# Kernel optimization log

Measured on AMD Instinct MI355X. Metric: run time of the kernel, lower is better.

## Reference

```python
import jax, jax.numpy as jnp
import numpy as np

D, H, HD, FF, L, SYM, B = 256, 8, 32, 256, 3, 64, 32768


def setup_inputs() -> dict:
    key = jax.random.key(0)
    ks = iter(jax.random.split(key, 32))
    n = lambda shape, s=0.02: jax.random.normal(next(ks), shape, dtype=jnp.float32) * s
    return {
        "global_emb": n((B, D), 1.0),
        "pert_emb": n((B, D), 1.0),
        "sym_feat": n((B, SYM), 1.0),
        "ppi_feat": n((B, D), 1.0),
        "sym_W": n((SYM, D)),
        "sym_b": jnp.zeros((D,), jnp.float32),
        "sym_ln_g": jnp.ones((D,), jnp.float32),
        "sym_ln_b": jnp.zeros((D,), jnp.float32),
        "token_type_emb": n((4, D)),
        "Wqkv": n((L, D, 3 * D)),
        "bqkv": jnp.zeros((L, 3 * D), jnp.float32),
        "Wo": n((L, D, D)),
        "bo": jnp.zeros((L, D), jnp.float32),
        "ln1_g": jnp.ones((L, D), jnp.float32),
        "ln1_b": jnp.zeros((L, D), jnp.float32),
        "ln2_g": jnp.ones((L, D), jnp.float32),
        "ln2_b": jnp.zeros((L, D), jnp.float32),
        "W1": n((L, D, FF)),
        "b1": jnp.zeros((L, FF), jnp.float32),
        "W2": n((L, FF, D)),
        "b2": jnp.zeros((L, D), jnp.float32),
        "final_ln_g": jnp.ones((D,), jnp.float32),
        "final_ln_b": jnp.zeros((D,), jnp.float32),
        "out_ln_g": jnp.ones((D,), jnp.float32),
        "out_ln_b": jnp.zeros((D,), jnp.float32),
    }


def _ln(x, g, b, eps=1e-5):
    m = jnp.mean(x, axis=-1, keepdims=True)
    v = jnp.mean(jnp.square(x - m), axis=-1, keepdims=True)
    return (x - m) * jax.lax.rsqrt(v + eps) * g + b


def reference(global_emb, pert_emb, sym_feat, ppi_feat, sym_W, sym_b, sym_ln_g,
              sym_ln_b, token_type_emb, Wqkv, bqkv, Wo, bo, ln1_g, ln1_b,
              ln2_g, ln2_b, W1, b1, W2, b2, final_ln_g, final_ln_b,
              out_ln_g, out_ln_b):
    # sym projection + LN, then stack 4 tokens and add token-type embedding
    sym_proj = _ln(sym_feat @ sym_W + sym_b, sym_ln_g, sym_ln_b)
    x = jnp.stack([global_emb, pert_emb, sym_proj, ppi_feat], axis=1)  # [B,4,D]
    x = x + token_type_emb[None]
    Bsz = x.shape[0]
    scale = 1.0 / np.sqrt(HD).astype(np.float32)
    for l in range(L):  # pre-norm TransformerEncoderLayer x3 (eval: dropout off)
        h = _ln(x, ln1_g[l], ln1_b[l])
        qkv = h @ Wqkv[l] + bqkv[l]  # [B,4,3D]
        q, k, v = jnp.split(qkv, 3, axis=-1)
        q = q.reshape(Bsz, 4, H, HD).transpose(0, 2, 1, 3)  # [B,H,4,HD]
        k = k.reshape(Bsz, 4, H, HD).transpose(0, 2, 1, 3)
        v = v.reshape(Bsz, 4, H, HD).transpose(0, 2, 1, 3)
        attn = jax.nn.softmax(jnp.einsum("bhqd,bhkd->bhqk", q, k) * scale, axis=-1)
        o = jnp.einsum("bhqk,bhkd->bhqd", attn, v)
        o = o.transpose(0, 2, 1, 3).reshape(Bsz, 4, D)
        x = x + (o @ Wo[l] + bo[l])
        h2 = _ln(x, ln2_g[l], ln2_b[l])
        ff = jax.nn.gelu(h2 @ W1[l] + b1[l], approximate=False) @ W2[l] + b2[l]
        x = x + ff
    x = _ln(x, final_ln_g, final_ln_b)  # TransformerEncoder final norm
    return _ln(jnp.mean(x, axis=1), out_ln_g, out_ln_b)  # mean over 4 tokens + out_norm
```

## Files before the change

kernel.cpp:

```cpp
#include <hip/hip_runtime.h>
#include <hip/hip_bf16.h>
#include <math.h>

typedef unsigned short u16;
typedef __attribute__((ext_vector_type(8))) short v8s;
typedef __attribute__((ext_vector_type(4))) short v4s;
typedef __attribute__((ext_vector_type(4))) float v4f;

__device__ __forceinline__ float bf2f(u16 u){
  union { float f; unsigned int i; } v; v.i = ((unsigned int)u) << 16; return v.f;
}
__device__ __forceinline__ u16 f2bf(float f){
  union { __hip_bfloat16 h; u16 u; } cv; cv.h = __float2bfloat16(f); return cv.u;
}
__device__ __forceinline__ bool det_bf16(const void* p){
  return ((const u16*)p)[0] != 0;
}
__device__ __forceinline__ float ldp(const void* p, size_t i, bool bf){
  return bf ? bf2f(((const u16*)p)[i]) : ((const float*)p)[i];
}
__device__ __forceinline__ void ld8f(const void* p, size_t i, bool bf, float* o){
  if (bf){
    v8s a = *(const v8s*)((const u16*)p + i);
    #pragma unroll
    for (int j=0;j<8;j++) o[j]=bf2f((u16)a[j]);
  } else {
    const float4* q=(const float4*)((const float*)p + i);
    float4 a=q[0], b=q[1];
    o[0]=a.x;o[1]=a.y;o[2]=a.z;o[3]=a.w;o[4]=b.x;o[5]=b.y;o[6]=b.z;o[7]=b.w;
  }
}
__device__ __forceinline__ void ld4f(const void* p, size_t i, bool bf, float* o){
  if (bf){
    v4s a = *(const v4s*)((const u16*)p + i);
    #pragma unroll
    for (int j=0;j<4;j++) o[j]=bf2f((u16)a[j]);
  } else {
    float4 q = *(const float4*)((const float*)p + i);
    o[0]=q.x;o[1]=q.y;o[2]=q.z;o[3]=q.w;
  }
}

#define MFMA(a,b,c) __builtin_amdgcn_mfma_f32_16x16x32_bf16((a),(b),(c),0,0,0)

template<int CTRL>
__device__ __forceinline__ float dpp_qp(float x){
  union { float f; int i; } u; u.f = x;
  u.i = __builtin_amdgcn_mov_dpp(u.i, CTRL, 0xF, 0xF, true);
  return u.f;
}

__device__ __forceinline__ int swz(int row, int col, int stride){
  return row*stride + ((((col>>3) ^ (row&7))<<3) | (col&7));
}

__device__ __forceinline__ void st4(u16* dst, v4f a, const float* b){
  v4s o;
  #pragma unroll
  for (int i=0;i<4;i++) o[i] = (short)f2bf(a[i] + b[i]);
  *(v4s*)dst = o;
}
__device__ __forceinline__ void rmw4(u16* p, v4f a, const float* b){
  v4s x = *(v4s*)p; v4s o;
  #pragma unroll
  for (int i=0;i<4;i++) o[i] = (short)f2bf(bf2f((u16)x[i]) + a[i] + b[i]);
  *(v4s*)p = o;
}

__device__ __forceinline__ float gelu_f(float u){
  float ax = fabsf(u)*0.70710678118f;
  float t = 1.f/(1.f + 0.3275911f*ax);
  float y = t*(0.254829592f + t*(-0.284496736f + t*(1.421413741f +
            t*(-1.453152027f + t*1.061405429f))));
  float er = 1.f - y*__expf(-ax*ax);
  er = copysignf(er, u);
  return 0.5f*u*(1.f + er);
}

__global__ __launch_bounds__(64) void repack_kernel(
    const void* __restrict__ symW, const void* __restrict__ Wqkv,
    const void* __restrict__ Wo, const void* __restrict__ W1, const void* __restrict__ W2,
    const void* __restrict__ ln1g, const void* __restrict__ ln1b,
    const void* __restrict__ ln2g, const void* __restrict__ ln2b,
    const void* __restrict__ bqkv, const void* __restrict__ b1,
    u16* __restrict__ wf_sym, u16* __restrict__ wf_qkv, u16* __restrict__ wf_o,
    u16* __restrict__ wf_1, u16* __restrict__ wf_2,
    float* __restrict__ cq1, float* __restrict__ cq0,
    float* __restrict__ cf1, float* __restrict__ cf0,
    const void* __restrict__ dtp)
{
  bool bf = det_bf16(dtp);
  int idx = blockIdx.x;
  int ln = threadIdx.x;

  if (idx >= 2336){
    int i2 = idx - 2336;
    int lay = i2 >> 4, r2 = i2 & 15;
    const void *Wp, *g, *be, *bb; size_t woff, goff, boff; int N, n; float *o1, *o0;
    if (r2 < 12){
      n = r2*64 + ln; N = 768; Wp = Wqkv; woff = (size_t)lay*196608;
      g = ln1g; be = ln1b; bb = bqkv; goff = (size_t)lay*256; boff = (size_t)lay*768;
      o1 = cq1 + lay*768; o0 = cq0 + lay*768;
    } else {
      int rr = r2 - 12; n = rr*64 + ln; N = 256; Wp = W1; woff = (size_t)lay*65536;
      g = ln2g; be = ln2b; bb = b1; goff = (size_t)lay*256; boff = (size_t)lay*256;
      o1 = cf1 + lay*256; o0 = cf0 + lay*256;
    }
    float a1 = 0.f, a0 = 0.f;
    for (int k = 0; k < 256; k++){
      float wv = ldp(Wp, woff + (size_t)k*N + n, bf);
      a1 += bf2f(f2bf(ldp(g, goff+k, bf) * wv));
      a0 += ldp(be, goff+k, bf) * wv;
    }
    o1[n] = a1;
    o0[n] = a0 + ldp(bb, boff + n, bf);
    return;
  }

  const void* src; u16* dst; int N, kb, nb; size_t soff;
  const void* gscale = nullptr; size_t gsoff = 0;
  if (idx < 32) { src = symW; dst = wf_sym; N = 256; kb = idx >> 4; nb = idx & 15; soff = 0; }
  else {
    idx -= 32;
    int lay = idx / 768, r = idx % 768;
    if (r < 384) { N = 768; src = Wqkv; soff = (size_t)lay*196608; dst = wf_qkv + lay*196608; kb = r/48; nb = r%48;
                   gscale = ln1g; gsoff = (size_t)lay*256; }
    else {
      r -= 384; int which = r >> 7, rr = r & 127; N = 256; kb = rr >> 4; nb = rr & 15;
      soff = (size_t)lay*65536;
      if (which == 0)      { src = Wo; dst = wf_o + lay*65536; }
      else if (which == 1) { src = W1; dst = wf_1 + lay*65536; gscale = ln2g; gsoff = (size_t)lay*256; }
      else                 { src = W2; dst = wf_2 + lay*65536; }
    }
  }
  int n  = nb*16 + (ln & 15);
  int k0 = kb*32 + (ln >> 4)*8;
  u16* d = dst + (((size_t)(kb*(N>>4) + nb))*64 + ln)*8;
  #pragma unroll
  for (int j = 0; j < 8; j++){
    float sc = gscale ? ldp(gscale, gsoff + k0 + j, bf) : 1.f;
    d[j] = f2bf(sc * ldp(src, soff + (size_t)(k0+j)*N + n, bf));
  }
}

__device__ __forceinline__ void ln64s(const u16* src, u16* dst,
    const void* gp, const void* bp, size_t goff, bool bf, int t)
{
  int r = t>>3, p = t&7;
  float vv[32];
  float su=0.f, sq=0.f;
  #pragma unroll
  for (int k4=0;k4<4;k4++){
    v8s a = *(const v8s*)(src + swz(r, p*32+k4*8, 256));
    #pragma unroll
    for (int j=0;j<8;j++){ float v=bf2f((u16)a[j]); vv[k4*8+j]=v; su+=v; sq+=v*v; }
  }
  su += dpp_qp<0xB1>(su); sq += dpp_qp<0xB1>(sq);
  su += dpp_qp<0x4E>(su); sq += dpp_qp<0x4E>(sq);
  su += __shfl_xor(su,4); sq += __shfl_xor(sq,4);
  float m = su*(1.f/256.f);
  float rs = rsqrtf(sq*(1.f/256.f) - m*m + 1e-5f);
  #pragma unroll
  for (int k4=0;k4<4;k4++){
    float gg[8], bb[8];
    ld8f(gp, goff + p*32 + k4*8, bf, gg);
    ld8f(bp, goff + p*32 + k4*8, bf, bb);
    v8s o;
    #pragma unroll
    for (int j=0;j<8;j++) o[j]=(short)f2bf((vv[k4*8+j]-m)*rs*gg[j]+bb[j]);
    *(v8s*)(dst + swz(r, p*32+k4*8, 256)) = o;
  }
}

__device__ __forceinline__ void mrs64(const u16* src, float* dst, int t){
  int r = t>>3, p = t&7;
  float su=0.f, sq=0.f;
  #pragma unroll
  for (int k4=0;k4<4;k4++){
    v8s a = *(const v8s*)(src + swz(r, p*32+k4*8, 256));
    #pragma unroll
    for (int j=0;j<8;j++){ float v=bf2f((u16)a[j]); su+=v; sq+=v*v; }
  }
  su += dpp_qp<0xB1>(su); sq += dpp_qp<0xB1>(sq);
  su += dpp_qp<0x4E>(su); sq += dpp_qp<0x4E>(sq);
  su += __shfl_xor(su,4); sq += __shfl_xor(sq,4);
  float m = su*(1.f/256.f);
  float rs = rsqrtf(sq*(1.f/256.f) - m*m + 1e-5f);
  if (p == 0){ dst[2*r] = m; dst[2*r+1] = rs; }
}

__global__ __launch_bounds__(512,4) void fused_kernel(
    const void* __restrict__ gemb, const void* __restrict__ pemb,
    const void* __restrict__ symf, const void* __restrict__ ppi,
    const void* __restrict__ symb, const void* __restrict__ slng,
    const void* __restrict__ slnb, const void* __restrict__ tte,
    const void* __restrict__ bo, const void* __restrict__ b2p,
    const void* __restrict__ flng, const void* __restrict__ flnb,
    const void* __restrict__ olng, const void* __restrict__ olnb,
    const float* __restrict__ cq1, const float* __restrict__ cq0,
    const float* __restrict__ cf1, const float* __restrict__ cf0,
    const u16* __restrict__ wf_sym, const u16* __restrict__ wf_qkv,
    const u16* __restrict__ wf_o, const u16* __restrict__ wf_1,
    const u16* __restrict__ wf_2,
    void* __restrict__ out)
{
  __shared__ __align__(16) u16 X[16384];
  __shared__ __align__(16) u16 H[16384];
  __shared__ __align__(16) u16 symst[1024];
  __shared__ __align__(8)  float mrsA[128];
  __shared__ __align__(8)  float mrsB[128];

  bool bf = det_bf16(slng);
  int t = threadIdx.x;
  int w = t>>6, ln = t&63, quad = ln>>4, c = ln&15;
  int row0 = blockIdx.x * 64;
  int S0 = row0 >> 2;

  {
    if (t < 128){
      int r = t>>3, pp = t&7;
      float tmp[8];
      ld8f(symf, (size_t)(S0+r)*64 + pp*8, bf, tmp);
      v8s o;
      #pragma unroll
      for (int j=0;j<8;j++) o[j]=(short)f2bf(tmp[j]);
      *(v8s*)(symst + swz(r, pp*8, 64)) = o;
    } else {
      int u = t-128;
      int rid = u>>3, p = u&7;
      int s = rid/3, z = rid - s*3;
      int tok = (z==2)?3:z;
      const void* src = (z==0)?gemb: (z==1)?pemb: ppi;
      #pragma unroll
      for (int k4=0;k4<4;k4++){
        float a8[8], t8[8];
        ld8f(src, (size_t)(S0+s)*256 + p*32 + k4*8, bf, a8);
        ld8f(tte, (size_t)tok*256 + p*32 + k4*8, bf, t8);
        v8s o;
        #pragma unroll
        for (int j=0;j<8;j++) o[j]=(short)f2bf(a8[j]+t8[j]);
        *(v8s*)(X + swz(s*4+tok, p*32+k4*8, 256)) = o;
      }
    }
    __syncthreads();
    {
      v4f acc[2];
      v4f z4={0.f,0.f,0.f,0.f};
      acc[0]=z4; acc[1]=z4;
      #pragma unroll
      for (int kb=0;kb<2;kb++){
        v8s a = *(const v8s*)(symst + swz(c, kb*32+quad*8, 64));
        #pragma unroll
        for (int j=0;j<2;j++){
          v8s b = *(const v8s*)(wf_sym + (((size_t)(kb*16+w*2+j))*64+ln)*8);
          acc[j] = MFMA(b, a, acc[j]);
        }
      }
      #pragma unroll
      for (int j=0;j<2;j++){
        int colb = (w*2+j)*16 + quad*4;
        float sb[4]; ld4f(symb, colb, bf, sb);
        st4(H + swz(c, colb, 256), acc[j], sb);
      }
    }
    __syncthreads();
    if (t < 128){
      int r = t>>3, p = t&7;
      float vv[32];
      float su=0.f, sq=0.f;
      #pragma unroll
      for (int k4=0;k4<4;k4++){
        v8s a = *(const v8s*)(H + swz(r, p*32+k4*8, 256));
        #pragma unroll
        for (int j=0;j<8;j++){ float v=bf2f((u16)a[j]); vv[k4*8+j]=v; su+=v; sq+=v*v; }
      }
      su += dpp_qp<0xB1>(su); sq += dpp_qp<0xB1>(sq);
      su += dpp_qp<0x4E>(su); sq += dpp_qp<0x4E>(sq);
      su += __shfl_xor(su,4); sq += __shfl_xor(sq,4);
      float m = su*(1.f/256.f);
      float rs = rsqrtf(sq*(1.f/256.f) - m*m + 1e-5f);
      #pragma unroll
      for (int k4=0;k4<4;k4++){
        float gg[8], bb[8], t8[8];
        ld8f(slng, p*32+k4*8, bf, gg);
        ld8f(slnb, p*32+k4*8, bf, bb);
        ld8f(tte, 512 + p*32+k4*8, bf, t8);
        v8s o;
        #pragma unroll
        for (int j=0;j<8;j++) o[j]=(short)f2bf((vv[k4*8+j]-m)*rs*gg[j]+bb[j]+t8[j]);
        *(v8s*)(X + swz(r*4+2, p*32+k4*8, 256)) = o;
      }
    }
    __syncthreads();
  }

  #pragma unroll 1
  for (int lay = 0; lay < 3; lay++){

    mrs64(X, mrsA, t);

    {
      const u16* wq = wf_qkv + (size_t)lay*196608;
      int h = w;
      v4f z4={0.f,0.f,0.f,0.f};
      const float scl = 0.17677669529663687f;
      v4f s01[2], s23[2];
      auto qkdots = [&](int hf, v4f* sout){
        v4f Qa[2][2], Ka[2][2];
        #pragma unroll
        for (int m2=0;m2<2;m2++){ Qa[m2][0]=z4;Qa[m2][1]=z4;Ka[m2][0]=z4;Ka[m2][1]=z4; }
        #pragma unroll 2
        for (int kb=0;kb<8;kb++){
          v8s Bq0 = *(const v8s*)(wq + (((size_t)(kb*48      + h*2  ))*64+ln)*8);
          v8s Bq1 = *(const v8s*)(wq + (((size_t)(kb*48      + h*2+1))*64+ln)*8);
          v8s Bk0 = *(const v8s*)(wq + (((size_t)(kb*48 + 16 + h*2  ))*64+ln)*8);
          v8s Bk1 = *(const v8s*)(wq + (((size_t)(kb*48 + 16 + h*2+1))*64+ln)*8);
          #pragma unroll
          for (int m2=0;m2<2;m2++){
            v8s a = *(const v8s*)(X + swz((hf*2+m2)*16+c, kb*32+quad*8, 256));
            Qa[m2][0]=MFMA(Bq0,a,Qa[m2][0]);
            Qa[m2][1]=MFMA(Bq1,a,Qa[m2][1]);
            Ka[m2][0]=MFMA(Bk0,a,Ka[m2][0]);
            Ka[m2][1]=MFMA(Bk1,a,Ka[m2][1]);
          }
        }
        if (hf == 0) __syncthreads();
        v4f q1[2], q0[2], k1[2], k0f[2];
        #pragma unroll
        for (int jj=0;jj<2;jj++){
          int d0 = lay*768 + h*32 + jj*16 + quad*4;
          q1[jj]  = *(const v4f*)(cq1 + d0);
          q0[jj]  = *(const v4f*)(cq0 + d0);
          k1[jj]  = *(const v4f*)(cq1 + d0 + 256);
          k0f[jj] = *(const v4f*)(cq0 + d0 + 256);
        }
        #pragma unroll
        for (int m2=0;m2<2;m2++){
          float2 mr = *(const float2*)&mrsA[2*((hf*2+m2)*16 + c)];
          float q8[8], k8[8];
          #pragma unroll
          for (int jj=0;jj<2;jj++)
            #pragma unroll
            for (int i=0;i<4;i++){
              q8[jj*4+i] = mr.y*(Qa[m2][jj][i] - mr.x*q1[jj][i]) + q0[jj][i];
              k8[jj*4+i] = mr.y*(Ka[m2][jj][i] - mr.x*k1[jj][i]) + k0f[jj][i];
            }
          float sp0=0.f, sp1=0.f, sp2=0.f, sp3=0.f;
          #pragma unroll
          for (int x=0;x<8;x++){
            sp0 += q8[x]*k8[x];
            sp1 += q8[x]*dpp_qp<0xB1>(k8[x]);
            sp2 += q8[x]*dpp_qp<0x4E>(k8[x]);
            sp3 += q8[x]*dpp_qp<0x1B>(k8[x]);
          }
          sp0 += __shfl_xor(sp0,16); sp0 += __shfl_xor(sp0,32);
          sp1 += __shfl_xor(sp1,16); sp1 += __shfl_xor(sp1,32);
          sp2 += __shfl_xor(sp2,16); sp2 += __shfl_xor(sp2,32);
          sp3 += __shfl_xor(sp3,16); sp3 += __shfl_xor(sp3,32);
          v4f s; s[0]=sp0*scl; s[1]=sp1*scl; s[2]=sp2*scl; s[3]=sp3*scl;
          sout[m2] = s;
        }
      };
      qkdots(0, s01);
      __builtin_amdgcn_sched_barrier(0);
      qkdots(1, s23);
      v4f p0, p1, p2, p3;
      {
        auto smax = [&](v4f s)->v4f{
          float mx = fmaxf(fmaxf(s[0],s[1]),fmaxf(s[2],s[3]));
          float e0=__expf(s[0]-mx), e1=__expf(s[1]-mx), e2=__expf(s[2]-mx), e3=__expf(s[3]-mx);
          float inv = 1.f/(e0+e1+e2+e3);
          v4f p; p[0]=e0*inv; p[1]=e1*inv; p[2]=e2*inv; p[3]=e3*inv;
          return p;
        };
        p0 = smax(s01[0]); p1 = smax(s01[1]); p2 = smax(s23[0]); p3 = smax(s23[1]);
      }
      v4f Va[4][2];
      #pragma unroll
      for (int mb=0;mb<4;mb++){ Va[mb][0]=z4; Va[mb][1]=z4; }
      #pragma unroll 2
      for (int kb=0;kb<8;kb++){
        v8s Bv0 = *(const v8s*)(wq + (((size_t)(kb*48 + 32 + h*2  ))*64+ln)*8);
        v8s Bv1 = *(const v8s*)(wq + (((size_t)(kb*48 + 32 + h*2+1))*64+ln)*8);
        #pragma unroll
        for (int mb=0;mb<4;mb++){
          v8s a = *(const v8s*)(X + swz(mb*16+c, kb*32+quad*8, 256));
          Va[mb][0]=MFMA(Bv0,a,Va[mb][0]);
          Va[mb][1]=MFMA(Bv1,a,Va[mb][1]);
        }
      }
      {
        v4f v1[2], v0[2];
        #pragma unroll
        for (int jj=0;jj<2;jj++){
          int d0 = lay*768 + 512 + h*32 + jj*16 + quad*4;
          v1[jj] = *(const v4f*)(cq1 + d0);
          v0[jj] = *(const v4f*)(cq0 + d0);
        }
        #pragma unroll
        for (int mb=0;mb<4;mb++){
          float2 mr = *(const float2*)&mrsA[2*(mb*16 + c)];
          #pragma unroll
          for (int jj=0;jj<2;jj++)
            #pragma unroll
            for (int i=0;i<4;i++)
              Va[mb][jj][i] = mr.y*(Va[mb][jj][i] - mr.x*v1[jj][i]) + v0[jj][i];
        }
      }
      #pragma unroll
      for (int mb=0;mb<4;mb++){
        v4f P = (mb==0)?p0:(mb==1)?p1:(mb==2)?p2:p3;
        #pragma unroll
        for (int jj=0;jj<2;jj++){
          v4f o;
          #pragma unroll
          for (int i=0;i<4;i++){
            float v = Va[mb][jj][i];
            float r = P[0]*v;
            r += P[1]*dpp_qp<0xB1>(v);
            r += P[2]*dpp_qp<0x4E>(v);
            r += P[3]*dpp_qp<0x1B>(v);
            o[i] = r;
          }
          v4s pk;
          #pragma unroll
          for (int i=0;i<4;i++) pk[i]=(short)f2bf(o[i]);
          *(v4s*)(H + swz(mb*16+c, h*32 + jj*16 + quad*4, 256)) = pk;
        }
      }
    }
    __syncthreads();

    {
      const u16* wo = wf_o + (size_t)lay*65536;
      v4f acc[4][2];
      v4f z4={0.f,0.f,0.f,0.f};
      #pragma unroll
      for (int mb=0;mb<4;mb++){ acc[mb][0]=z4; acc[mb][1]=z4; }
      #pragma unroll 2
      for (int kb=0;kb<8;kb++){
        v8s B0 = *(const v8s*)(wo + (((size_t)(kb*16 + w*2  ))*64+ln)*8);
        v8s B1 = *(const v8s*)(wo + (((size_t)(kb*16 + w*2+1))*64+ln)*8);
        #pragma unroll
        for (int mb=0;mb<4;mb++){
          v8s a = *(const v8s*)(H + swz(mb*16+c, kb*32+quad*8, 256));
          acc[mb][0]=MFMA(B0,a,acc[mb][0]);
          acc[mb][1]=MFMA(B1,a,acc[mb][1]);
        }
      }
      #pragma unroll
      for (int jj=0;jj<2;jj++){
        int colb = (w*2+jj)*16 + quad*4;
        float bs[4]; ld4f(bo, (size_t)lay*256 + colb, bf, bs);
        #pragma unroll
        for (int mb=0;mb<4;mb++)
          rmw4(X + swz(mb*16+c, colb, 256), acc[mb][jj], bs);
      }
    }
    __syncthreads();

    mrs64(X, mrsB, t);

    {
      const u16* w1 = wf_1 + (size_t)lay*65536;
      v4f acc[4][2];
      v4f z4={0.f,0.f,0.f,0.f};
      #pragma unroll
      for (int mb=0;mb<4;mb++){ acc[mb][0]=z4; acc[mb][1]=z4; }
      #pragma unroll 2
      for (int kb=0;kb<8;kb++){
        v8s B0 = *(const v8s*)(w1 + (((size_t)(kb*16 + w*2  ))*64+ln)*8);
        v8s B1 = *(const v8s*)(w1 + (((size_t)(kb*16 + w*2+1))*64+ln)*8);
        #pragma unroll
        for (int mb=0;mb<4;mb++){
          v8s a = *(const v8s*)(X + swz(mb*16+c, kb*32+quad*8, 256));
          acc[mb][0]=MFMA(B0,a,acc[mb][0]);
          acc[mb][1]=MFMA(B1,a,acc[mb][1]);
        }
      }
      __syncthreads();
      #pragma unroll
      for (int jj=0;jj<2;jj++){
        int colb = (w*2+jj)*16 + quad*4;
        v4f f1 = *(const v4f*)(cf1 + lay*256 + colb);
        v4f f0 = *(const v4f*)(cf0 + lay*256 + colb);
        #pragma unroll
        for (int mb=0;mb<4;mb++){
          float2 mr = *(const float2*)&mrsB[2*(mb*16 + c)];
          v4s pk;
          #pragma unroll
          for (int i=0;i<4;i++){
            float val = mr.y*(acc[mb][jj][i] - mr.x*f1[i]) + f0[i];
            pk[i]=(short)f2bf(gelu_f(val));
          }
          *(v4s*)(H + swz(mb*16+c, colb, 256)) = pk;
        }
      }
    }
    __syncthreads();

    {
      const u16* w2 = wf_2 + (size_t)lay*65536;
      v4f acc[4][2];
      v4f z4={0.f,0.f,0.f,0.f};
      #pragma unroll
      for (int mb=0;mb<4;mb++){ acc[mb][0]=z4; acc[mb][1]=z4; }
      #pragma unroll 2
      for (int kb=0;kb<8;kb++){
        v8s B0 = *(const v8s*)(w2 + (((size_t)(kb*16 + w*2  ))*64+ln)*8);
        v8s B1 = *(const v8s*)(w2 + (((size_t)(kb*16 + w*2+1))*64+ln)*8);
        #pragma unroll
        for (int mb=0;mb<4;mb++){
          v8s a = *(const v8s*)(H + swz(mb*16+c, kb*32+quad*8, 256));
          acc[mb][0]=MFMA(B0,a,acc[mb][0]);
          acc[mb][1]=MFMA(B1,a,acc[mb][1]);
        }
      }
      #pragma unroll
      for (int jj=0;jj<2;jj++){
        int colb = (w*2+jj)*16 + quad*4;
        float bs[4]; ld4f(b2p, (size_t)lay*256 + colb, bf, bs);
        #pragma unroll
        for (int mb=0;mb<4;mb++)
          rmw4(X + swz(mb*16+c, colb, 256), acc[mb][jj], bs);
      }
    }
    __syncthreads();
  }

  ln64s(X, H, flng, flnb, 0, bf, t);
  __syncthreads();
  if (t < 128){
    int s = t>>3, p = t&7;
    float y[32];
    #pragma unroll
    for (int j=0;j<32;j++) y[j]=0.f;
    #pragma unroll
    for (int r4=0;r4<4;r4++)
      #pragma unroll
      for (int k4=0;k4<4;k4++){
        v8s a = *(const v8s*)(H + swz(s*4+r4, p*32+k4*8, 256));
        #pragma unroll
        for (int j=0;j<8;j++) y[k4*8+j] += bf2f((u16)a[j]);
      }
    float su=0.f, sq=0.f;
    #pragma unroll
    for (int j=0;j<32;j++){ y[j]*=0.25f; su+=y[j]; sq+=y[j]*y[j]; }
    su += dpp_qp<0xB1>(su); sq += dpp_qp<0xB1>(sq);
    su += dpp_qp<0x4E>(su); sq += dpp_qp<0x4E>(sq);
    su += __shfl_xor(su,4); sq += __shfl_xor(sq,4);
    float m = su*(1.f/256.f);
    float rs = rsqrtf(sq*(1.f/256.f) - m*m + 1e-5f);
    #pragma unroll
    for (int k4=0;k4<4;k4++){
      float gg[8], bb[8];
      ld8f(olng, p*32+k4*8, bf, gg);
      ld8f(olnb, p*32+k4*8, bf, bb);
      if (bf){
        u16* dst = (u16*)out + (size_t)(S0+s)*256 + p*32 + k4*8;
        v8s o;
        #pragma unroll
        for (int j=0;j<8;j++) o[j]=(short)f2bf((y[k4*8+j]-m)*rs*gg[j]+bb[j]);
        *(v8s*)dst = o;
      } else {
        float* dst = (float*)out + (size_t)(S0+s)*256 + p*32 + k4*8;
        #pragma unroll
        for (int j=0;j<8;j++) dst[j] = (y[k4*8+j]-m)*rs*gg[j]+bb[j];
      }
    }
  }
}

extern "C" void kernel_launch(void* const* d_in, const int* in_sizes, int n_in,
                              void* d_out, int out_size, void* d_ws, size_t ws_size,
                              hipStream_t stream)
{
  const void* gemb=d_in[0];
  const void* pemb=d_in[1];
  const void* symf=d_in[2];
  const void* ppi =d_in[3];
  const void* symW=d_in[4];
  const void* symb=d_in[5];
  const void* slng=d_in[6];
  const void* slnb=d_in[7];
  const void* tte =d_in[8];
  const void* Wqkv=d_in[9];
  const void* bqkv=d_in[10];
  const void* Wo  =d_in[11];
  const void* bo  =d_in[12];
  const void* ln1g=d_in[13];
  const void* ln1b=d_in[14];
  const void* ln2g=d_in[15];
  const void* ln2b=d_in[16];
  const void* W1  =d_in[17];
  const void* b1  =d_in[18];
  const void* W2  =d_in[19];
  const void* b2  =d_in[20];
  const void* flng=d_in[21];
  const void* flnb=d_in[22];
  const void* olng=d_in[23];
  const void* olnb=d_in[24];

  u16* wf_sym=(u16*)d_ws;
  u16* wf_qkv=wf_sym + 16384;
  u16* wf_o  =wf_qkv + 589824;
  u16* wf_1  =wf_o  + 196608;
  u16* wf_2  =wf_1  + 196608;
  float* cq1 = (float*)(wf_2 + 196608);
  float* cq0 = cq1 + 2304;
  float* cf1 = cq0 + 2304;
  float* cf0 = cf1 + 768;

  repack_kernel<<<2384,64,0,stream>>>(symW,Wqkv,Wo,W1,W2,
      ln1g,ln1b,ln2g,ln2b,bqkv,b1,
      wf_sym,wf_qkv,wf_o,wf_1,wf_2, cq1,cq0,cf1,cf0, slng);
  fused_kernel<<<2048,512,0,stream>>>(
      gemb,pemb,symf,ppi,symb,slng,slnb,tte,bo,b2,
      flng,flnb,olng,olnb, cq1,cq0,cf1,cf0,
      wf_sym,wf_qkv,wf_o,wf_1,wf_2, d_out);
}
```

Baseline: 727.8 us.

## Halve block tile to 32 rows with 4 waves, each wave covering more columns

After: 1.033 ms. 41.9% more time.

```diff
diff --git a/kernel.cpp b/kernel.cpp
--- a/kernel.cpp
+++ b/kernel.cpp
@@ -143,7 +143,7 @@
   }
 }
 
-__device__ __forceinline__ void ln64s(const u16* src, u16* dst,
+__device__ __forceinline__ void ln32s(const u16* src, u16* dst,
     const void* gp, const void* bp, size_t goff, bool bf, int t)
 {
   int r = t>>3, p = t&7;
@@ -172,7 +172,7 @@
   }
 }
 
-__device__ __forceinline__ void mrs64(const u16* src, float* dst, int t){
+__device__ __forceinline__ void mrs32(const u16* src, float* dst, int t){
   int r = t>>3, p = t&7;
   float su=0.f, sq=0.f;
   #pragma unroll
@@ -189,7 +189,7 @@
   if (p == 0){ dst[2*r] = m; dst[2*r+1] = rs; }
 }
 
-__global__ __launch_bounds__(512,4) void fused_kernel(
+__global__ __launch_bounds__(256,4) void fused_kernel(
     const void* __restrict__ gemb, const void* __restrict__ pemb,
     const void* __restrict__ symf, const void* __restrict__ ppi,
     const void* __restrict__ symb, const void* __restrict__ slng,
@@ -204,20 +204,20 @@
     const u16* __restrict__ wf_2,
     void* __restrict__ out)
 {
-  __shared__ __align__(16) u16 X[16384];
-  __shared__ __align__(16) u16 H[16384];
+  __shared__ __align__(16) u16 X[8192];
+  __shared__ __align__(16) u16 H[8192];
   __shared__ __align__(16) u16 symst[1024];
-  __shared__ __align__(8)  float mrsA[128];
-  __shared__ __align__(8)  float mrsB[128];
+  __shared__ __align__(8)  float mrsA[64];
+  __shared__ __align__(8)  float mrsB[64];
 
   bool bf = det_bf16(slng);
   int t = threadIdx.x;
   int w = t>>6, ln = t&63, quad = ln>>4, c = ln&15;
-  int row0 = blockIdx.x * 64;
+  int row0 = blockIdx.x * 32;
   int S0 = row0 >> 2;
 
   {
-    if (t < 128){
+    if (t < 64){
       int r = t>>3, pp = t&7;
       float tmp[8];
       ld8f(symf, (size_t)(S0+r)*64 + pp*8, bf, tmp);
@@ -226,7 +226,7 @@
       for (int j=0;j<8;j++) o[j]=(short)f2bf(tmp[j]);
       *(v8s*)(symst + swz(r, pp*8, 64)) = o;
     } else {
-      int u = t-128;
+      int u = t-64;
       int rid = u>>3, p = u&7;
       int s = rid/3, z = rid - s*3;
       int tok = (z==2)?3:z;
@@ -244,27 +244,30 @@
     }
     __syncthreads();
     {
-      v4f acc[2];
+      v4f acc[4];
       v4f z4={0.f,0.f,0.f,0.f};
-      acc[0]=z4; acc[1]=z4;
+      #pragma unroll
+      for (int j=0;j<4;j++) acc[j]=z4;
       #pragma unroll
       for (int kb=0;kb<2;kb++){
         v8s a = *(const v8s*)(symst + swz(c, kb*32+quad*8, 64));
         #pragma unroll
-        for (int j=0;j<2;j++){
-          v8s b = *(const v8s*)(wf_sym + (((size_t)(kb*16+w*2+j))*64+ln)*8);
+        for (int j=0;j<4;j++){
+          v8s b = *(const v8s*)(wf_sym + (((size_t)(kb*16+w*4+j))*64+ln)*8);
           acc[j] = MFMA(b, a, acc[j]);
         }
       }
-      #pragma unroll
-      for (int j=0;j<2;j++){
-        int colb = (w*2+j)*16 + quad*4;
-        float sb[4]; ld4f(symb, colb, bf, sb);
-        st4(H + swz(c, colb, 256), acc[j], sb);
+      if (c < 8){
+        #pragma unroll
+        for (int j=0;j<4;j++){
+          int colb = (w*4+j)*16 + quad*4;
+          float sb[4]; ld4f(symb, colb, bf, sb);
+          st4(H + swz(c, colb, 256), acc[j], sb);
+        }
       }
     }
     __syncthreads();
-    if (t < 128){
+    if (t < 64){
       int r = t>>3, p = t&7;
       float vv[32];
       float su=0.f, sq=0.f;
@@ -297,15 +300,14 @@
   #pragma unroll 1
   for (int lay = 0; lay < 3; lay++){
 
-    mrs64(X, mrsA, t);
+    mrs32(X, mrsA, t);
 
     {
       const u16* wq = wf_qkv + (size_t)lay*196608;
-      int h = w;
       v4f z4={0.f,0.f,0.f,0.f};
       const float scl = 0.17677669529663687f;
-      v4f s01[2], s23[2];
-      auto qkdots = [&](int hf, v4f* sout){
+      v4f s0h[2], s1h[2];
+      auto qkdots = [&](int h, bool bar, v4f* sout){
         v4f Qa[2][2], Ka[2][2];
         #pragma unroll
         for (int m2=0;m2<2;m2++){ Qa[m2][0]=z4;Qa[m2][1]=z4;Ka[m2][0]=z4;Ka[m2][1]=z4; }
@@ -317,14 +319,14 @@
           v8s Bk1 = *(const v8s*)(wq + (((size_t)(kb*48 + 16 + h*2+1))*64+ln)*8);
           #pragma unroll
           for (int m2=0;m2<2;m2++){
-            v8s a = *(const v8s*)(X + swz((hf*2+m2)*16+c, kb*32+quad*8, 256));
+            v8s a = *(const v8s*)(X + swz(m2*16+c, kb*32+quad*8, 256));
             Qa[m2][0]=MFMA(Bq0,a,Qa[m2][0]);
             Qa[m2][1]=MFMA(Bq1,a,Qa[m2][1]);
             Ka[m2][0]=MFMA(Bk0,a,Ka[m2][0]);
             Ka[m2][1]=MFMA(Bk1,a,Ka[m2][1]);
           }
         }
-        if (hf == 0) __syncthreads();
+        if (bar) __syncthreads();
         v4f q1[2], q0[2], k1[2], k0f[2];
         #pragma unroll
         for (int jj=0;jj<2;jj++){
@@ -336,7 +338,7 @@
         }
         #pragma unroll
         for (int m2=0;m2<2;m2++){
-          float2 mr = *(const float2*)&mrsA[2*((hf*2+m2)*16 + c)];
+          float2 mr = *(const float2*)&mrsA[2*(m2*16 + c)];
           float q8[8], k8[8];
           #pragma unroll
           for (int jj=0;jj<2;jj++)
@@ -361,10 +363,10 @@
           sout[m2] = s;
         }
       };
-      qkdots(0, s01);
+      qkdots(w*2+0, true,  s0h);
       __builtin_amdgcn_sched_barrier(0);
-      qkdots(1, s23);
-      v4f p0, p1, p2, p3;
+      qkdots(w*2+1, false, s1h);
+      v4f p00, p01, p10, p11;
       {
         auto smax = [&](v4f s)->v4f{
           float mx = fmaxf(fmaxf(s[0],s[1]),fmaxf(s[2],s[3]));
@@ -373,23 +375,34 @@
           v4f p; p[0]=e0*inv; p[1]=e1*inv; p[2]=e2*inv; p[3]=e3*inv;
           return p;
         };
-        p0 = smax(s01[0]); p1 = smax(s01[1]); p2 = smax(s23[0]); p3 = smax(s23[1]);
-      }
-      v4f Va[4][2];
-      #pragma unroll
-      for (int mb=0;mb<4;mb++){ Va[mb][0]=z4; Va[mb][1]=z4; }
+        p00 = smax(s0h[0]); p01 = smax(s0h[1]); p10 = smax(s1h[0]); p11 = smax(s1h[1]);
+      }
+      v4f Va[2][2][2];
+      #pragma unroll
+      for (int hh=0;hh<2;hh++)
+        #pragma unroll
+        for (int mb=0;mb<2;mb++){ Va[hh][mb][0]=z4; Va[hh][mb][1]=z4; }
       #pragma unroll 2
       for (int kb=0;kb<8;kb++){
-        v8s Bv0 = *(const v8s*)(wq + (((size_t)(kb*48 + 32 + h*2  ))*64+ln)*8);
-        v8s Bv1 = *(const v8s*)(wq + (((size_t)(kb*48 + 32 + h*2+1))*64+ln)*8);
-        #pragma unroll
-        for (int mb=0;mb<4;mb++){
+        v8s Bv[2][2];
+        #pragma unroll
+        for (int hh=0;hh<2;hh++)
+          #pragma unroll
+          for (int jj=0;jj<2;jj++)
+            Bv[hh][jj] = *(const v8s*)(wq + (((size_t)(kb*48 + 32 + (w*2+hh)*2+jj))*64+ln)*8);
+        #pragma unroll
+        for (int mb=0;mb<2;mb++){
           v8s a = *(const v8s*)(X + swz(mb*16+c, kb*32+quad*8, 256));
-          Va[mb][0]=MFMA(Bv0,a,Va[mb][0]);
-          Va[mb][1]=MFMA(Bv1,a,Va[mb][1]);
-        }
-      }
-      {
+          #pragma unroll
+          for (int hh=0;hh<2;hh++){
+            Va[hh][mb][0]=MFMA(Bv[hh][0],a,Va[hh][mb][0]);
+            Va[hh][mb][1]=MFMA(Bv[hh][1],a,Va[hh][mb][1]);
+          }
+        }
+      }
+      #pragma unroll
+      for (int hh=0;hh<2;hh++){
+        int h = w*2+hh;
         v4f v1[2], v0[2];
         #pragma unroll
         for (int jj=0;jj<2;jj++){
@@ -398,34 +411,26 @@
           v0[jj] = *(const v4f*)(cq0 + d0);
         }
         #pragma unroll
-        for (int mb=0;mb<4;mb++){
+        for (int mb=0;mb<2;mb++){
           float2 mr = *(const float2*)&mrsA[2*(mb*16 + c)];
-          #pragma unroll
-          for (int jj=0;jj<2;jj++)
+          v4f P = (hh==0) ? ((mb==0)?p00:p01) : ((mb==0)?p10:p11);
+          #pragma unroll
+          for (int jj=0;jj<2;jj++){
+            v4f o;
             #pragma unroll
-            for (int i=0;i<4;i++)
-              Va[mb][jj][i] = mr.y*(Va[mb][jj][i] - mr.x*v1[jj][i]) + v0[jj][i];
-        }
-      }
-      #pragma unroll
-      for (int mb=0;mb<4;mb++){
-        v4f P = (mb==0)?p0:(mb==1)?p1:(mb==2)?p2:p3;
-        #pragma unroll
-        for (int jj=0;jj<2;jj++){
-          v4f o;
-          #pragma unroll
-          for (int i=0;i<4;i++){
-            float v = Va[mb][jj][i];
-            float r = P[0]*v;
-            r += P[1]*dpp_qp<0xB1>(v);
-            r += P[2]*dpp_qp<0x4E>(v);
-            r += P[3]*dpp_qp<0x1B>(v);
-            o[i] = r;
+            for (int i=0;i<4;i++){
+              float v = mr.y*(Va[hh][mb][jj][i] - mr.x*v1[jj][i]) + v0[jj][i];
+              float r = P[0]*v;
+              r += P[1]*dpp_qp<0xB1>(v);
+              r += P[2]*dpp_qp<0x4E>(v);
+              r += P[3]*dpp_qp<0x1B>(v);
+              o[i] = r;
+            }
+            v4s pk;
+            #pragma unroll
+            for (int i=0;i<4;i++) pk[i]=(short)f2bf(o[i]);
+            *(v4s*)(H + swz(mb*16+c, h*32 + jj*16 + quad*4, 256)) = pk;
           }
-          v4s pk;
-          #pragma unroll
-          for (int i=0;i<4;i++) pk[i]=(short)f2bf(o[i]);
-          *(v4s*)(H + swz(mb*16+c, h*32 + jj*16 + quad*4, 256)) = pk;
         }
       }
     }
@@ -433,59 +438,67 @@
 
     {
       const u16* wo = wf_o + (size_t)lay*65536;
-      v4f acc[4][2];
+      v4f acc[2][4];
       v4f z4={0.f,0.f,0.f,0.f};
       #pragma unroll
-      for (int mb=0;mb<4;mb++){ acc[mb][0]=z4; acc[mb][1]=z4; }
+      for (int mb=0;mb<2;mb++)
+        #pragma unroll
+        for (int j=0;j<4;j++) acc[mb][j]=z4;
       #pragma unroll 2
       for (int kb=0;kb<8;kb++){
-        v8s B0 = *(const v8s*)(wo + (((size_t)(kb*16 + w*2  ))*64+ln)*8);
-        v8s B1 = *(const v8s*)(wo + (((size_t)(kb*16 + w*2+1))*64+ln)*8);
-        #pragma unroll
-        for (int mb=0;mb<4;mb++){
+        v8s B[4];
+        #pragma unroll
+        for (int j=0;j<4;j++)
+          B[j] = *(const v8s*)(wo + (((size_t)(kb*16 + w*4+j))*64+ln)*8);
+        #pragma unroll
+        for (int mb=0;mb<2;mb++){
           v8s a = *(const v8s*)(H + swz(mb*16+c, kb*32+quad*8, 256));
-          acc[mb][0]=MFMA(B0,a,acc[mb][0]);
-          acc[mb][1]=MFMA(B1,a,acc[mb][1]);
-        }
-      }
-      #pragma unroll
-      for (int jj=0;jj<2;jj++){
-        int colb = (w*2+jj)*16 + quad*4;
+          #pragma unroll
+          for (int j=0;j<4;j++) acc[mb][j]=MFMA(B[j],a,acc[mb][j]);
+        }
+      }
+      #pragma unroll
+      for (int jj=0;jj<4;jj++){
+        int colb = (w*4+jj)*16 + quad*4;
         float bs[4]; ld4f(bo, (size_t)lay*256 + colb, bf, bs);
         #pragma unroll
-        for (int mb=0;mb<4;mb++)
+        for (int mb=0;mb<2;mb++)
           rmw4(X + swz(mb*16+c, colb, 256), acc[mb][jj], bs);
       }
     }
     __syncthreads();
 
-    mrs64(X, mrsB, t);
+    mrs32(X, mrsB, t);
 
     {
       const u16* w1 = wf_1 + (size_t)lay*65536;
-      v4f acc[4][2];
+      v4f acc[2][4];
       v4f z4={0.f,0.f,0.f,0.f};
       #pragma unroll
-      for (int mb=0;mb<4;mb++){ acc[mb][0]=z4; acc[mb][1]=z4; }
+      for (int mb=0;mb<2;mb++)
+        #pragma unroll
+        for (int j=0;j<4;j++) acc[mb][j]=z4;
       #pragma unroll 2
       for (int kb=0;kb<8;kb++){
-        v8s B0 = *(const v8s*)(w1 + (((size_t)(kb*16 + w*2  ))*64+ln)*8);
-        v8s B1 = *(const v8s*)(w1 + (((size_t)(kb*16 + w*2+1))*64+ln)*8);
-        #pragma unroll
-        for (int mb=0;mb<4;mb++){
+        v8s B[4];
+        #pragma unroll
+        for (int j=0;j<4;j++)
+          B[j] = *(const v8s*)(w1 + (((size_t)(kb*16 + w*4+j))*64+ln)*8);
+        #pragma unroll
+        for (int mb=0;mb<2;mb++){
           v8s a = *(const v8s*)(X + swz(mb*16+c, kb*32+quad*8, 256));
-          acc[mb][0]=MFMA(B0,a,acc[mb][0]);
-          acc[mb][1]=MFMA(B1,a,acc[mb][1]);
+          #pragma unroll
+          for (int j=0;j<4;j++) acc[mb][j]=MFMA(B[j],a,acc[mb][j]);
         }
       }
       __syncthreads();
       #pragma unroll
-      for (int jj=0;jj<2;jj++){
-        int colb = (w*2+jj)*16 + quad*4;
+      for (int jj=0;jj<4;jj++){
+        int colb = (w*4+jj)*16 + quad*4;
         v4f f1 = *(const v4f*)(cf1 + lay*256 + colb);
         v4f f0 = *(const v4f*)(cf0 + lay*256 + colb);
         #pragma unroll
-        for (int mb=0;mb<4;mb++){
+        for (int mb=0;mb<2;mb++){
           float2 mr = *(const float2*)&mrsB[2*(mb*16 + c)];
           v4s pk;
           #pragma unroll
@@ -501,36 +514,40 @@
 
     {
       const u16* w2 = wf_2 + (size_t)lay*65536;
-      v4f acc[4][2];
+      v4f acc[2][4];
       v4f z4={0.f,0.f,0.f,0.f};
       #pragma unroll
-      for (int mb=0;mb<4;mb++){ acc[mb][0]=z4; acc[mb][1]=z4; }
+      for (int mb=0;mb<2;mb++)
+        #pragma unroll
+        for (int j=0;j<4;j++) acc[mb][j]=z4;
       #pragma unroll 2
       for (int kb=0;kb<8;kb++){
-        v8s B0 = *(const v8s*)(w2 + (((size_t)(kb*16 + w*2  ))*64+ln)*8);
-        v8s B1 = *(const v8s*)(w2 + (((size_t)(kb*16 + w*2+1))*64+ln)*8);
-        #pragma unroll
-        for (int mb=0;mb<4;mb++){
+        v8s B[4];
+        #pragma unroll
+        for (int j=0;j<4;j++)
+          B[j] = *(const v8s*)(w2 + (((size_t)(kb*16 + w*4+j))*64+ln)*8);
+        #pragma unroll
+        for (int mb=0;mb<2;mb++){
           v8s a = *(const v8s*)(H + swz(mb*16+c, kb*32+quad*8, 256));
-          acc[mb][0]=MFMA(B0,a,acc[mb][0]);
-          acc[mb][1]=MFMA(B1,a,acc[mb][1]);
-        }
-      }
-      #pragma unroll
-      for (int jj=0;jj<2;jj++){
-        int colb = (w*2+jj)*16 + quad*4;
+          #pragma unroll
+          for (int j=0;j<4;j++) acc[mb][j]=MFMA(B[j],a,acc[mb][j]);
+        }
+      }
+      #pragma unroll
+      for (int jj=0;jj<4;jj++){
+        int colb = (w*4+jj)*16 + quad*4;
         float bs[4]; ld4f(b2p, (size_t)lay*256 + colb, bf, bs);
         #pragma unroll
-        for (int mb=0;mb<4;mb++)
+        for (int mb=0;mb<2;mb++)
           rmw4(X + swz(mb*16+c, colb, 256), acc[mb][jj], bs);
       }
     }
     __syncthreads();
   }
 
-  ln64s(X, H, flng, flnb, 0, bf, t);
+  ln32s(X, H, flng, flnb, 0, bf, t);
   __syncthreads();
-  if (t < 128){
+  if (t < 64){
     int s = t>>3, p = t&7;
     float y[32];
     #pragma unroll
@@ -614,7 +631,7 @@
   repack_kernel<<<2384,64,0,stream>>>(symW,Wqkv,Wo,W1,W2,
       ln1g,ln1b,ln2g,ln2b,bqkv,b1,
       wf_sym,wf_qkv,wf_o,wf_1,wf_2, cq1,cq0,cf1,cf0, slng);
-  fused_kernel<<<2048,512,0,stream>>>(
+  fused_kernel<<<4096,256,0,stream>>>(
       gemb,pemb,symf,ppi,symb,slng,slnb,tte,bo,b2,
       flng,flnb,olng,olnb, cq1,cq0,cf1,cf0,
       wf_sym,wf_qkv,wf_o,wf_1,wf_2, d_out);
```
